# Kernel tuning notes

Hardware: AMD Instinct MI355X
Metric: run time of the kernel (lower is better)

## Reference

```python
import jax, jax.numpy as jnp
import numpy as np

ALPHA = 0.2  # LeakyReLU negative slope
N, F_IN, F_OUT = 8192, 512, 64
NEG_INF = -9e15


def setup_inputs() -> dict:
    key = jax.random.key(0)
    k1, k2, k3, k4 = jax.random.split(key, 4)
    inp = jax.random.normal(k1, (N, F_IN), dtype=jnp.float32)
    adj = jax.random.randint(k2, (N, N), 0, 2, dtype=jnp.int32)
    W = jax.random.normal(k3, (F_IN, F_OUT), dtype=jnp.float32) * (1.414 / np.sqrt(F_IN))
    a = jax.random.normal(k4, (2 * F_OUT, 1), dtype=jnp.float32) * 0.1
    return {"input": inp, "adj": adj, "W": W, "a": a, "sparse": 0}


def reference(input, adj, W, a, sparse):
    h = input @ W  # [N, F_out]
    # Decompose concat([h_i, h_j]) @ a into additive src/dst terms (same math,
    # avoids the O(N^2 * 2F) intermediate): e_ij = leakyrelu(h_i@a1 + h_j@a2)
    f_src = h @ a[:F_OUT]   # [N, 1]
    f_dst = h @ a[F_OUT:]   # [N, 1]
    e = jax.nn.leaky_relu(f_src + f_dst.T, ALPHA)  # [N, N]
    attention = jnp.where(adj > 0, e, NEG_INF)
    attention = jax.nn.softmax(attention, axis=1)
    h_prime = attention @ h  # [N, F_out]
    return jax.nn.leaky_relu(h_prime, 0.01)[None]  # concat=True path; default F.leaky_relu slope 0.01
```

## Files before the change

### kernel.cpp

```cpp
#include <hip/hip_runtime.h>
#include <hip/hip_bf16.h>

#define N 8192
#define FIN 512
#define FOUT 64
#define ALPHA 0.2f

typedef __bf16 bf16x8 __attribute__((ext_vector_type(8)));
typedef __bf16 bf16x4 __attribute__((ext_vector_type(4)));
typedef float f32x4 __attribute__((ext_vector_type(4)));
typedef int i32x4 __attribute__((ext_vector_type(4)));

constexpr int JCH = 256;
constexpr int CPB = 4;
constexpr int NCH = 8;
constexpr int HSTR = JCH + 8;


__device__ __forceinline__ unsigned enc_f(float x) {
    unsigned u = __float_as_uint(x);
    return (u & 0x80000000u) ? ~u : (u | 0x80000000u);
}
__device__ __forceinline__ float dec_f(unsigned u) {
    return (u & 0x80000000u) ? __uint_as_float(u & 0x7FFFFFFFu) : __uint_as_float(~u);
}

__global__ __launch_bounds__(64) void k_wt(const float* __restrict__ W,
                                           __bf16* __restrict__ WtG) {
    const int g = blockIdx.x * 64 + threadIdx.x;
    const int k = g >> 3;
    const int f0 = (g & 7) * 8;
    const float4 w0 = *(const float4*)(W + (size_t)k * FOUT + f0);
    const float4 w1 = *(const float4*)(W + (size_t)k * FOUT + f0 + 4);
    WtG[(size_t)(f0 + 0) * FIN + k] = (__bf16)w0.x;
    WtG[(size_t)(f0 + 1) * FIN + k] = (__bf16)w0.y;
    WtG[(size_t)(f0 + 2) * FIN + k] = (__bf16)w0.z;
    WtG[(size_t)(f0 + 3) * FIN + k] = (__bf16)w0.w;
    WtG[(size_t)(f0 + 4) * FIN + k] = (__bf16)w1.x;
    WtG[(size_t)(f0 + 5) * FIN + k] = (__bf16)w1.y;
    WtG[(size_t)(f0 + 6) * FIN + k] = (__bf16)w1.z;
    WtG[(size_t)(f0 + 7) * FIN + k] = (__bf16)w1.w;
}

__global__ __launch_bounds__(64) void k12(const float* __restrict__ in,
                                          const __bf16* __restrict__ WtG,
                                          const float* __restrict__ a,
                                          float* __restrict__ f_src,
                                          float* __restrict__ f_dst,
                                          unsigned* __restrict__ Mkey,
                                          __bf16* __restrict__ hT) {
    __shared__ __bf16 tb[64][16];
    const int lane = threadIdx.x;
    const int m = lane & 15, quad = lane >> 4;
    const int i0 = blockIdx.x * 16;

    f32x4 acc[4];
#pragma unroll
    for (int t = 0; t < 4; ++t) acc[t] = (f32x4){0.f, 0.f, 0.f, 0.f};

    const float* arow = in + (size_t)(i0 + m) * FIN + quad * 8;
    for (int k0 = 0; k0 < FIN; k0 += 32) {
        const float4 x0 = *(const float4*)(arow + k0);
        const float4 x1 = *(const float4*)(arow + k0 + 4);
        bf16x8 af;
        af[0] = (__bf16)x0.x; af[1] = (__bf16)x0.y; af[2] = (__bf16)x0.z; af[3] = (__bf16)x0.w;
        af[4] = (__bf16)x1.x; af[5] = (__bf16)x1.y; af[6] = (__bf16)x1.z; af[7] = (__bf16)x1.w;
#pragma unroll
        for (int t = 0; t < 4; ++t) {
            const bf16x8 bf = *(const bf16x8*)(WtG + (size_t)(t * 16 + m) * FIN + k0 + quad * 8);
            acc[t] = __builtin_amdgcn_mfma_f32_16x16x32_bf16(af, bf, acc[t], 0, 0, 0);
        }
    }
    float s1[4], s2[4];
#pragma unroll
    for (int r = 0; r < 4; ++r) { s1[r] = 0.f; s2[r] = 0.f; }
#pragma unroll
    for (int t = 0; t < 4; ++t) {
        const float a1 = a[t * 16 + m], a2 = a[64 + t * 16 + m];
#pragma unroll
        for (int r = 0; r < 4; ++r) {
            s1[r] += acc[t][r] * a1;
            s2[r] += acc[t][r] * a2;
        }
    }
#pragma unroll
    for (int off = 1; off <= 8; off <<= 1)
#pragma unroll
        for (int r = 0; r < 4; ++r) {
            s1[r] += __shfl_xor(s1[r], off);
            s2[r] += __shfl_xor(s2[r], off);
        }
    float lm = -1e30f;
    if (m == 0) {
#pragma unroll
        for (int r = 0; r < 4; ++r) {
            f_src[i0 + quad * 4 + r] = s1[r];
            f_dst[i0 + quad * 4 + r] = s2[r];
            lm = fmaxf(lm, s2[r]);
        }
    }
    lm = fmaxf(lm, __shfl_xor(lm, 16));
    lm = fmaxf(lm, __shfl_xor(lm, 32));
    if (lane == 0) atomicMax(Mkey, enc_f(lm));

#pragma unroll
    for (int t = 0; t < 4; ++t)
#pragma unroll
        for (int r = 0; r < 4; ++r) tb[t * 16 + m][quad * 4 + r] = (__bf16)acc[t][r];
    __syncthreads();
    {
        const int f = lane;
        const bf16x8 v0 = *(const bf16x8*)&tb[f][0];
        const bf16x8 v1 = *(const bf16x8*)&tb[f][8];
        *(bf16x8*)(hT + (size_t)f * N + i0) = v0;
        *(bf16x8*)(hT + (size_t)f * N + i0 + 8) = v1;
    }
}

__global__ __launch_bounds__(256) void k3_attn(const int* __restrict__ adj,
                                               const float* __restrict__ f_src,
                                               const float* __restrict__ fdstG,
                                               const unsigned* __restrict__ Mkey,
                                               const __bf16* __restrict__ hT,
                                               float* __restrict__ pnum,
                                               float* __restrict__ plsum) {
    __shared__ __bf16 sh[64 * HSTR];
    __shared__ __bf16 wlds[4 * 16 * HSTR];
    const int tid = threadIdx.x;
    const int wv = tid >> 6, lane = tid & 63;
    const int m = lane & 15, quad = lane >> 4;
    const int i0w = (blockIdx.x * 4 + wv) * 16;
    const int jb = blockIdx.y * (JCH * CPB);
    const float LOG2E = 1.44269504088896f;
    const int wbase = wv * 16 * HSTR;

    const float M = dec_f(*Mkey);
    float fsr_a[16], shr_a[16];
#pragma unroll
    for (int r = 0; r < 16; ++r) {
        const float fsr = f_src[i0w + r];
        const float tt = fsr + M;
        fsr_a[r] = fsr;
        shr_a[r] = fmaxf(tt, ALPHA * tt);
    }

    f32x4 acc[4];
#pragma unroll
    for (int t = 0; t < 4; ++t) acc[t] = (f32x4){0.f, 0.f, 0.f, 0.f};
    f32x4 accl = (f32x4){0.f, 0.f, 0.f, 0.f};

    bf16x8 bones;
#pragma unroll
    for (int jj = 0; jj < 8; ++jj) bones[jj] = (__bf16)(m == 0 ? 1.0f : 0.0f);

    for (int c = 0; c < CPB; ++c) {
        const int jc = jb + c * JCH;
        __syncthreads();

#pragma unroll
        for (int k = 0; k < 8; ++k) {
            const int s = tid + k * 256;
            const int f = s >> 5, off = (s & 31) * 8;
            *(bf16x8*)&sh[f * HSTR + off] = *(const bf16x8*)(hT + (size_t)f * N + jc + off);
        }

        const f32x4 fd = *(const f32x4*)(fdstG + jc + lane * 4);
#pragma unroll
        for (int r = 0; r < 16; ++r) {
            const i32x4 am = __builtin_nontemporal_load(
                (const i32x4*)(adj + (size_t)(i0w + r) * N + jc + lane * 4));
            const float fsr = fsr_a[r], sh_r = shr_a[r];
            bf16x4 w4;
#pragma unroll
            for (int jj = 0; jj < 4; ++jj) {
                float e = fsr + fd[jj];
                e = fmaxf(e, ALPHA * e);
                const float ex = __builtin_amdgcn_exp2f((e - sh_r) * LOG2E);
                w4[jj] = (__bf16)(am[jj] > 0 ? ex : 0.f);
            }
            *(bf16x4*)&wlds[wbase + r * HSTR + lane * 4] = w4;
        }
        __syncthreads();

#pragma unroll
        for (int s = 0; s < 8; ++s) {
            const bf16x8 af = *(const bf16x8*)&wlds[wbase + m * HSTR + s * 32 + quad * 8];
#pragma unroll
            for (int t = 0; t < 4; ++t) {
                const bf16x8 bfr = *(const bf16x8*)&sh[(t * 16 + m) * HSTR + s * 32 + quad * 8];
                acc[t] = __builtin_amdgcn_mfma_f32_16x16x32_bf16(af, bfr, acc[t], 0, 0, 0);
            }
            accl = __builtin_amdgcn_mfma_f32_16x16x32_bf16(af, bones, accl, 0, 0, 0);
        }
    }

    float* pn = pnum + (size_t)blockIdx.y * N * FOUT;
#pragma unroll
    for (int t = 0; t < 4; ++t)
#pragma unroll
        for (int r = 0; r < 4; ++r)
            pn[(size_t)(i0w + quad * 4 + r) * FOUT + t * 16 + m] = acc[t][r];
    if (m == 0) {
#pragma unroll
        for (int r = 0; r < 4; ++r)
            plsum[(size_t)blockIdx.y * N + i0w + quad * 4 + r] = accl[r];
    }
}

__global__ __launch_bounds__(256) void k4_norm(const float* __restrict__ pnum,
                                               const float* __restrict__ plsum,
                                               float* __restrict__ out) {
    const int idx = blockIdx.x * 256 + threadIdx.x;
    const int row = idx >> 6;
    float s = 0.f, l = 0.f;
#pragma unroll
    for (int c = 0; c < NCH; ++c) {
        s += pnum[(size_t)c * N * FOUT + idx];
        l += plsum[(size_t)c * N + row];
    }
    const float v = s / (l > 0.f ? l : 1.f);
    out[idx] = v > 0.f ? v : 0.01f * v;
}

extern "C" void kernel_launch(void* const* d_in, const int* in_sizes, int n_in,
                              void* d_out, int out_size, void* d_ws, size_t ws_size,
                              hipStream_t stream) {
    const float* in = (const float*)d_in[0];
    const int* adj = (const int*)d_in[1];
    const float* W = (const float*)d_in[2];
    const float* a = (const float*)d_in[3];
    float* out = (float*)d_out;

    char* ws = (char*)d_ws;
    unsigned* Mkey = (unsigned*)ws;
    float* f_src = (float*)(ws + 4096);
    float* f_dst = (float*)(ws + 36864);
    __bf16* WtG = (__bf16*)(ws + 69632);
    __bf16* hT = (__bf16*)(ws + 135168);
    float* plsum = (float*)(ws + 2097152);
    float* pnum = (float*)(ws + 4194304);

    hipMemsetAsync(ws, 0, 64, stream);

    k_wt<<<64, 64, 0, stream>>>(W, WtG);
    k12<<<N / 16, 64, 0, stream>>>(in, WtG, a, f_src, f_dst, Mkey, hT);

    dim3 g3(N / 64, NCH);
    k3_attn<<<g3, 256, 0, stream>>>(adj, f_src, f_dst, Mkey, hT, pnum, plsum);
    k4_norm<<<(N * FOUT) / 256, 256, 0, stream>>>(pnum, plsum, out);
}
```

Baseline: 465.7 us.

## Pack adjacency to bitmask and compute attention weights in registers with 64-row tiles

Adds a pre-pass that packs the int32 adjacency matrix into a bitmask. The attention kernel now reads mask bits and builds the bf16 A-fragments directly in registers instead of staging them through LDS. Each wave now handles 64 rows (four M-tiles), so every B fragment of h loaded from LDS is reused across four MFMA row tiles. The column split changes to 16 chunks of 512, which doubles the partial-sum traffic and the reduction work in k4_norm. The pack pass still reads the full 256MB adjacency once, and a wave now holds 80 accumulator registers, which raises register pressure.

```diff
diff --git a/kernel.cpp b/kernel.cpp
--- a/kernel.cpp
+++ b/kernel.cpp
@@ -7,14 +7,14 @@
 #define ALPHA 0.2f
 
 typedef __bf16 bf16x8 __attribute__((ext_vector_type(8)));
-typedef __bf16 bf16x4 __attribute__((ext_vector_type(4)));
 typedef float f32x4 __attribute__((ext_vector_type(4)));
 typedef int i32x4 __attribute__((ext_vector_type(4)));
 
 constexpr int JCH = 256;
-constexpr int CPB = 4;
-constexpr int NCH = 8;
+constexpr int CPB = 2;
+constexpr int NCH = 16;
 constexpr int HSTR = JCH + 8;
+constexpr int NW = N / 32;
 
 
 __device__ __forceinline__ unsigned enc_f(float x) {
@@ -42,6 +42,29 @@
     WtG[(size_t)(f0 + 7) * FIN + k] = (__bf16)w1.w;
 }
 
+__global__ __launch_bounds__(256) void k_pack(const int* __restrict__ adj,
+                                              unsigned* __restrict__ abit) {
+    const int lane = threadIdx.x & 63;
+    const int wg = blockIdx.x * 4 + (threadIdx.x >> 6);
+#pragma unroll
+    for (int rr = 0; rr < 2; ++rr) {
+        const int row = wg * 2 + rr;
+        const int* src = adj + (size_t)row * N;
+        unsigned* dst = abit + (size_t)row * NW;
+#pragma unroll 4
+        for (int c = 0; c < 32; ++c) {
+            const i32x4 v = *(const i32x4*)(src + c * 256 + lane * 4);
+            unsigned w = ((unsigned)(v[0] > 0) | ((unsigned)(v[1] > 0) << 1) |
+                          ((unsigned)(v[2] > 0) << 2) | ((unsigned)(v[3] > 0) << 3))
+                         << (4 * (lane & 7));
+            w |= __shfl_xor(w, 1);
+            w |= __shfl_xor(w, 2);
+            w |= __shfl_xor(w, 4);
+            if ((lane & 7) == 0) dst[c * 8 + (lane >> 3)] = w;
+        }
+    }
+}
+
 __global__ __launch_bounds__(64) void k12(const float* __restrict__ in,
                                           const __bf16* __restrict__ WtG,
                                           const float* __restrict__ a,
@@ -117,7 +140,7 @@
     }
 }
 
-__global__ __launch_bounds__(256) void k3_attn(const int* __restrict__ adj,
+__global__ __launch_bounds__(256) void k3_attn(const unsigned* __restrict__ abit,
                                                const float* __restrict__ f_src,
                                                const float* __restrict__ fdstG,
                                                const unsigned* __restrict__ Mkey,
@@ -125,29 +148,32 @@
                                                float* __restrict__ pnum,
                                                float* __restrict__ plsum) {
     __shared__ __bf16 sh[64 * HSTR];
-    __shared__ __bf16 wlds[4 * 16 * HSTR];
+    __shared__ float sfd[JCH * CPB];
     const int tid = threadIdx.x;
     const int wv = tid >> 6, lane = tid & 63;
     const int m = lane & 15, quad = lane >> 4;
-    const int i0w = (blockIdx.x * 4 + wv) * 16;
+    const int i0w = blockIdx.x * 256 + wv * 64;
     const int jb = blockIdx.y * (JCH * CPB);
     const float LOG2E = 1.44269504088896f;
-    const int wbase = wv * 16 * HSTR;
+
+    if (tid < (JCH * CPB) / 4) *(f32x4*)&sfd[tid * 4] = *(const f32x4*)(fdstG + jb + tid * 4);
 
     const float M = dec_f(*Mkey);
-    float fsr_a[16], shr_a[16];
-#pragma unroll
-    for (int r = 0; r < 16; ++r) {
-        const float fsr = f_src[i0w + r];
-        const float tt = fsr + M;
-        fsr_a[r] = fsr;
-        shr_a[r] = fmaxf(tt, ALPHA * tt);
-    }
-
-    f32x4 acc[4];
-#pragma unroll
-    for (int t = 0; t < 4; ++t) acc[t] = (f32x4){0.f, 0.f, 0.f, 0.f};
-    f32x4 accl = (f32x4){0.f, 0.f, 0.f, 0.f};
+    float fs[4], sht[4];
+#pragma unroll
+    for (int mt = 0; mt < 4; ++mt) {
+        fs[mt] = f_src[i0w + mt * 16 + m];
+        const float tt = fs[mt] + M;
+        sht[mt] = fmaxf(tt, ALPHA * tt);
+    }
+
+    f32x4 acc[4][4], accl[4];
+#pragma unroll
+    for (int mt = 0; mt < 4; ++mt) {
+        accl[mt] = (f32x4){0.f, 0.f, 0.f, 0.f};
+#pragma unroll
+        for (int t = 0; t < 4; ++t) acc[mt][t] = (f32x4){0.f, 0.f, 0.f, 0.f};
+    }
 
     bf16x8 bones;
 #pragma unroll
@@ -156,54 +182,56 @@
     for (int c = 0; c < CPB; ++c) {
         const int jc = jb + c * JCH;
         __syncthreads();
-
 #pragma unroll
         for (int k = 0; k < 8; ++k) {
             const int s = tid + k * 256;
             const int f = s >> 5, off = (s & 31) * 8;
             *(bf16x8*)&sh[f * HSTR + off] = *(const bf16x8*)(hT + (size_t)f * N + jc + off);
         }
-
-        const f32x4 fd = *(const f32x4*)(fdstG + jc + lane * 4);
-#pragma unroll
-        for (int r = 0; r < 16; ++r) {
-            const i32x4 am = __builtin_nontemporal_load(
-                (const i32x4*)(adj + (size_t)(i0w + r) * N + jc + lane * 4));
-            const float fsr = fsr_a[r], sh_r = shr_a[r];
-            bf16x4 w4;
-#pragma unroll
-            for (int jj = 0; jj < 4; ++jj) {
-                float e = fsr + fd[jj];
-                e = fmaxf(e, ALPHA * e);
-                const float ex = __builtin_amdgcn_exp2f((e - sh_r) * LOG2E);
-                w4[jj] = (__bf16)(am[jj] > 0 ? ex : 0.f);
+        __syncthreads();
+
+#pragma unroll
+        for (int s = 0; s < 8; ++s) {
+            const int widx = (jc >> 5) + s;
+            const f32x4 fd0 = *(const f32x4*)&sfd[c * JCH + s * 32 + quad * 8];
+            const f32x4 fd1 = *(const f32x4*)&sfd[c * JCH + s * 32 + quad * 8 + 4];
+            bf16x8 B[4];
+#pragma unroll
+            for (int t = 0; t < 4; ++t)
+                B[t] = *(const bf16x8*)&sh[(t * 16 + m) * HSTR + s * 32 + quad * 8];
+#pragma unroll
+            for (int mt = 0; mt < 4; ++mt) {
+                const unsigned mw = abit[(size_t)(i0w + mt * 16 + m) * NW + widx];
+                const unsigned bits = mw >> (quad * 8);
+                bf16x8 af;
+#pragma unroll
+                for (int jj = 0; jj < 8; ++jj) {
+                    float e = fs[mt] + (jj < 4 ? fd0[jj] : fd1[jj - 4]);
+                    e = fmaxf(e, ALPHA * e);
+                    const float ex = __builtin_amdgcn_exp2f((e - sht[mt]) * LOG2E);
+                    af[jj] = (__bf16)(((bits >> jj) & 1u) ? ex : 0.f);
+                }
+#pragma unroll
+                for (int t = 0; t < 4; ++t)
+                    acc[mt][t] = __builtin_amdgcn_mfma_f32_16x16x32_bf16(af, B[t], acc[mt][t], 0, 0, 0);
+                accl[mt] = __builtin_amdgcn_mfma_f32_16x16x32_bf16(af, bones, accl[mt], 0, 0, 0);
             }
-            *(bf16x4*)&wlds[wbase + r * HSTR + lane * 4] = w4;
-        }
-        __syncthreads();
-
-#pragma unroll
-        for (int s = 0; s < 8; ++s) {
-            const bf16x8 af = *(const bf16x8*)&wlds[wbase + m * HSTR + s * 32 + quad * 8];
-#pragma unroll
-            for (int t = 0; t < 4; ++t) {
-                const bf16x8 bfr = *(const bf16x8*)&sh[(t * 16 + m) * HSTR + s * 32 + quad * 8];
-                acc[t] = __builtin_amdgcn_mfma_f32_16x16x32_bf16(af, bfr, acc[t], 0, 0, 0);
-            }
-            accl = __builtin_amdgcn_mfma_f32_16x16x32_bf16(af, bones, accl, 0, 0, 0);
         }
     }
 
     float* pn = pnum + (size_t)blockIdx.y * N * FOUT;
 #pragma unroll
-    for (int t = 0; t < 4; ++t)
-#pragma unroll
-        for (int r = 0; r < 4; ++r)
-            pn[(size_t)(i0w + quad * 4 + r) * FOUT + t * 16 + m] = acc[t][r];
-    if (m == 0) {
-#pragma unroll
-        for (int r = 0; r < 4; ++r)
-            plsum[(size_t)blockIdx.y * N + i0w + quad * 4 + r] = accl[r];
+    for (int mt = 0; mt < 4; ++mt) {
+#pragma unroll
+        for (int t = 0; t < 4; ++t)
+#pragma unroll
+            for (int r = 0; r < 4; ++r)
+                pn[(size_t)(i0w + mt * 16 + quad * 4 + r) * FOUT + t * 16 + m] = acc[mt][t][r];
+        if (m == 0) {
+#pragma unroll
+            for (int r = 0; r < 4; ++r)
+                plsum[(size_t)blockIdx.y * N + i0w + mt * 16 + quad * 4 + r] = accl[mt][r];
+        }
     }
 }
 
@@ -237,15 +265,17 @@
     float* f_dst = (float*)(ws + 36864);
     __bf16* WtG = (__bf16*)(ws + 69632);
     __bf16* hT = (__bf16*)(ws + 135168);
-    float* plsum = (float*)(ws + 2097152);
-    float* pnum = (float*)(ws + 4194304);
+    unsigned* abit = (unsigned*)(ws + 1183744);
+    float* plsum = (float*)(ws + 16777216);
+    float* pnum = (float*)(ws + 20971520);
 
     hipMemsetAsync(ws, 0, 64, stream);
 
     k_wt<<<64, 64, 0, stream>>>(W, WtG);
+    k_pack<<<1024, 256, 0, stream>>>(adj, abit);
     k12<<<N / 16, 64, 0, stream>>>(in, WtG, a, f_src, f_dst, Mkey, hT);
 
-    dim3 g3(N / 64, NCH);
-    k3_attn<<<g3, 256, 0, stream>>>(adj, f_src, f_dst, Mkey, hT, pnum, plsum);
+    dim3 g3(N / 256, NCH);
+    k3_attn<<<g3, 256, 0, stream>>>(abit, f_src, f_dst, Mkey, hT, pnum, plsum);
     k4_norm<<<(N * FOUT) / 256, 256, 0, stream>>>(pnum, plsum, out);
 }
```

New measurement: 442.1 us. -5.1%, faster.
